# Kernel optimization log

Measured on AMD Instinct MI355X. Metric: run time of the kernel, lower is better.

The kernel has to match this reference:

```python
import jax, jax.numpy as jnp
import numpy as np

B, N, D, H, E = 8, 2048, 128, 256, 524288
EPS = 1e-5

def setup_inputs() -> dict:
    key = jax.random.key(0)
    ks = jax.random.split(key, 16)
    def lin(k, fan_in, shape):
        b = 1.0 / np.sqrt(fan_in)
        return jax.random.uniform(k, shape, jnp.float32, -b, b)
    return {
        'x': jax.random.normal(ks[0], (B, N, 3), jnp.float32),
        'h': jax.random.normal(ks[1], (B, N, D), jnp.float32),
        'edge_indices': jax.random.randint(ks[2], (2, E), 0, B * N, jnp.int64),
        'batch_size': B,
        # filter_net: Linear(1,H) -> SiLU -> Linear(H,D)   (weights stored [in,out])
        'W1': lin(ks[3], 1, (1, H)), 'b1': lin(ks[4], 1, (H,)),
        'W2': lin(ks[5], H, (H, D)), 'b2': lin(ks[6], H, (D,)),
        # update_net: Linear(2D,H) -> LayerNorm(H) -> SiLU -> Linear(H,D)
        'W3': lin(ks[7], 2 * D, (2 * D, H)), 'b3': lin(ks[8], 2 * D, (H,)),
        'gamma': jnp.ones((H,), jnp.float32), 'beta': jnp.zeros((H,), jnp.float32),
        'W4': lin(ks[9], H, (H, D)), 'b4': lin(ks[10], H, (D,)),
    }

def reference(x, h, edge_indices, batch_size, W1, b1, W2, b2, W3, b3, gamma, beta, W4, b4):
    Bn, Nn, Dn = h.shape
    row, col = edge_indices[0], edge_indices[1]
    br, nr = row // Nn, row % Nn
    bc, nc = col // Nn, col % Nn
    x_row = x[br, nr]            # [E,3] gather
    x_col = x[bc, nc]            # [E,3]
    h_col = h[bc, nc]            # [E,D]
    diff = x_row - x_col
    dist = jnp.sqrt(jnp.sum(diff * diff, axis=-1, keepdims=True))  # [E,1]
    # distance-conditioned edge filter MLP
    edge_filters = jax.nn.silu(dist @ W1 + b1) @ W2 + b2           # [E,D]
    messages = h_col * edge_filters                                 # [E,D]
    # scatter-mean into B*N nodes (single-pass sum + count, clamp_min(1))
    n_tot = Bn * Nn
    sums = jax.ops.segment_sum(messages, row, num_segments=n_tot)
    counts = jax.ops.segment_sum(jnp.ones_like(row, dtype=messages.dtype), row, num_segments=n_tot)
    agg = (sums / jnp.maximum(counts, 1.0)[:, None]).reshape(Bn, Nn, Dn)
    # update MLP with LayerNorm
    u = jnp.concatenate([h, agg], axis=-1) @ W3 + b3               # [B,N,H]
    mu = jnp.mean(u, axis=-1, keepdims=True)
    var = jnp.mean((u - mu) ** 2, axis=-1, keepdims=True)
    un = (u - mu) * jax.lax.rsqrt(var + EPS) * gamma + beta
    return jax.nn.silu(un) @ W4 + b4                                # [B,N,D]
```

## Files before the change

kernel.cpp:

```cpp
#include <hip/hip_runtime.h>
#include <hip/hip_fp16.h>
#include <math.h>

#define BN_NODES 16384
#define DIM 128
#define HID 256
#define TK 4096
#define TRANGE 32.0f
#define TSTEP (TRANGE / (float)TK)
#define TINV  ((float)TK / TRANGE)
#define LN_EPS 1e-5f
#define EPB 4096
#define NBINS 1024
#define CAPB 768

typedef _Float16 f16x8 __attribute__((ext_vector_type(8)));
typedef __attribute__((ext_vector_type(4))) float f32x4;
typedef __attribute__((ext_vector_type(2))) float floatx2;
typedef __attribute__((ext_vector_type(8))) unsigned short ushort8v;

__device__ __forceinline__ unsigned short f2h(float f) {
    _Float16 h = (_Float16)f;
    return *(unsigned short*)&h;
}
__device__ __forceinline__ unsigned char f2fp8(float f) {
    unsigned int p = __builtin_amdgcn_cvt_pk_fp8_f32(f, f, 0, false);
    return (unsigned char)(p & 0xFFu);
}

__device__ __forceinline__ void acc8(uint2 q, uint2 tv, float* a) {
    floatx2 h01 = __builtin_amdgcn_cvt_pk_f32_fp8((int)q.x, false);
    floatx2 h23 = __builtin_amdgcn_cvt_pk_f32_fp8((int)q.x, true);
    floatx2 h45 = __builtin_amdgcn_cvt_pk_f32_fp8((int)q.y, false);
    floatx2 h67 = __builtin_amdgcn_cvt_pk_f32_fp8((int)q.y, true);
    floatx2 t01 = __builtin_amdgcn_cvt_pk_f32_fp8((int)tv.x, false);
    floatx2 t23 = __builtin_amdgcn_cvt_pk_f32_fp8((int)tv.x, true);
    floatx2 t45 = __builtin_amdgcn_cvt_pk_f32_fp8((int)tv.y, false);
    floatx2 t67 = __builtin_amdgcn_cvt_pk_f32_fp8((int)tv.y, true);
    a[0] = fmaf(h01[0], t01[0], a[0]);
    a[1] = fmaf(h01[1], t01[1], a[1]);
    a[2] = fmaf(h23[0], t23[0], a[2]);
    a[3] = fmaf(h23[1], t23[1], a[3]);
    a[4] = fmaf(h45[0], t45[0], a[4]);
    a[5] = fmaf(h45[1], t45[1], a[5]);
    a[6] = fmaf(h67[0], t67[0], a[6]);
    a[7] = fmaf(h67[1], t67[1], a[7]);
}

__device__ __forceinline__ void edge_one(const unsigned int* lrec, int idx, int dd,
        const unsigned char* __restrict__ xq,
        const unsigned char* __restrict__ Tb, float* a) {
    unsigned int r0 = lrec[idx];
    int c0 = (int)((r0 >> 12) & 0x3FFFu), k0 = (int)(r0 & 0xFFFu);
    uint2 q0 = *(const uint2*)&xq[c0 * DIM + dd];
    uint2 t0 = *(const uint2*)&Tb[k0 * DIM + dd];
    acc8(q0, t0, a);
}

__global__ __launch_bounds__(256) void prep_kernel(
        const float* __restrict__ W1, const float* __restrict__ b1,
        const float* __restrict__ W2, const float* __restrict__ b2,
        const float* __restrict__ W3, const float* __restrict__ W4,
        const float* __restrict__ h, const int* __restrict__ ei,
        const float* __restrict__ x,
        unsigned char* __restrict__ Tb, unsigned short* __restrict__ w3t,
        unsigned short* __restrict__ w4t, unsigned short* __restrict__ xh,
        unsigned char* __restrict__ xq, int* __restrict__ bin_cursor,
        unsigned int* __restrict__ staging, int nE) {
    __shared__ float smem[8 * 256 + 8 * 128];
    int bid = blockIdx.x, t = threadIdx.x;
    if (bid < 512) {
        float* a    = smem;
        float* part = smem + 8 * 256;
        int k0 = bid * 8;
        float w1 = W1[t], bb = b1[t];
#pragma unroll
        for (int k = 0; k < 8; ++k) {
            float dist = ((float)(k0 + k) + 0.5f) * TSTEP;
            float z = dist * w1 + bb;
            a[k * 256 + t] = z / (1.0f + expf(-z));
        }
        __syncthreads();
        int hg = t >> 7, d = t & 127;
        float acc[8] = {0.f,0.f,0.f,0.f,0.f,0.f,0.f,0.f};
        for (int hh = 0; hh < 128; ++hh) {
            int hidx = hg * 128 + hh;
            float w = W2[hidx * DIM + d];
#pragma unroll
            for (int k = 0; k < 8; ++k) acc[k] += a[k * 256 + hidx] * w;
        }
        if (hg == 1) {
#pragma unroll
            for (int k = 0; k < 8; ++k) part[k * 128 + d] = acc[k];
        }
        __syncthreads();
        if (hg == 0) {
            float bd = b2[d];
#pragma unroll
            for (int k = 0; k < 8; ++k)
                Tb[(k0 + k) * DIM + d] = f2fp8(acc[k] + part[k * 128 + d] + bd);
        }
    } else if (bid < 576) {
        float* s = smem;
        int tid = bid - 512, tr = tid >> 3, tc = tid & 7;
        int lr = t >> 5, lc = t & 31;
#pragma unroll
        for (int rep = 0; rep < 4; ++rep) {
            int k = tr * 32 + rep * 8 + lr, n = tc * 32 + lc;
            s[lc * 33 + rep * 8 + lr] = W3[k * 256 + n];
        }
        __syncthreads();
#pragma unroll
        for (int rep = 0; rep < 4; ++rep) {
            int n = tc * 32 + rep * 8 + lr, k = tr * 32 + lc;
            w3t[n * 256 + k] = f2h(s[(rep * 8 + lr) * 33 + lc]);
        }
    } else if (bid < 608) {
        float* s = smem;
        int tid = bid - 576, tr = tid >> 2, tc = tid & 3;
        int lr = t >> 5, lc = t & 31;
#pragma unroll
        for (int rep = 0; rep < 4; ++rep) {
            int k = tr * 32 + rep * 8 + lr, n = tc * 32 + lc;
            s[lc * 33 + rep * 8 + lr] = W4[k * 128 + n];
        }
        __syncthreads();
#pragma unroll
        for (int rep = 0; rep < 4; ++rep) {
            int n = tc * 32 + rep * 8 + lr, k = tr * 32 + lc;
            w4t[n * 256 + k] = f2h(s[(rep * 8 + lr) * 33 + lc]);
        }
    } else if (bid < 1632) {
        int i0 = (bid - 608) * 2048 + t * 8;
        float4 v0 = *(const float4*)&h[i0];
        float4 v1 = *(const float4*)&h[i0 + 4];
        ushort8v o;
        o[0] = f2h(v0.x); o[1] = f2h(v0.y); o[2] = f2h(v0.z); o[3] = f2h(v0.w);
        o[4] = f2h(v1.x); o[5] = f2h(v1.y); o[6] = f2h(v1.z); o[7] = f2h(v1.w);
        *(ushort8v*)&xh[i0] = o;
        unsigned int q0 = 0, q1 = 0;
        q0 = __builtin_amdgcn_cvt_pk_fp8_f32(v0.x, v0.y, q0, false);
        q0 = __builtin_amdgcn_cvt_pk_fp8_f32(v0.z, v0.w, q0, true);
        q1 = __builtin_amdgcn_cvt_pk_fp8_f32(v1.x, v1.y, q1, false);
        q1 = __builtin_amdgcn_cvt_pk_fp8_f32(v1.z, v1.w, q1, true);
        uint2 qq; qq.x = q0; qq.y = q1;
        *(uint2*)&xq[i0] = qq;
    } else {
        __shared__ int cnt[NBINS];
        __shared__ int pre[NBINS];
        __shared__ int gba[NBINS];
        __shared__ int sc[256];
        __shared__ unsigned int rec[EPB];
        int e0 = (bid - 1632) * EPB;
        int m = min(EPB, nE - e0);
        if (m < 0) m = 0;
#pragma unroll
        for (int j = 0; j < 4; ++j) cnt[j * 256 + t] = 0;
        __syncthreads();
        unsigned int code[16];
        int rk[16], bn[16];
#pragma unroll
        for (int j = 0; j < 16; ++j) {
            int idx = j * 256 + t;
            rk[j] = -1; bn[j] = 0; code[j] = 0;
            if (idx < m) {
                int e = e0 + idx;
                int r = ei[e], c = ei[nE + e];
                code[j] = ((unsigned int)r << 14) | (unsigned int)c;
                bn[j] = r >> 4;
                rk[j] = atomicAdd(&cnt[bn[j]], 1);
            }
        }
        __syncthreads();
        int c4[4], s4 = 0;
#pragma unroll
        for (int j = 0; j < 4; ++j) { c4[j] = cnt[t * 4 + j]; s4 += c4[j]; }
        sc[t] = s4;
        __syncthreads();
        for (int off = 1; off < 256; off <<= 1) {
            int v = (t >= off) ? sc[t - off] : 0;
            __syncthreads();
            sc[t] += v;
            __syncthreads();
        }
        int run = sc[t] - s4;
#pragma unroll
        for (int j = 0; j < 4; ++j) {
            int b = t * 4 + j;
            pre[b] = run; run += c4[j];
            gba[b] = atomicAdd(&bin_cursor[b], c4[j]);
        }
        __syncthreads();
#pragma unroll
        for (int j = 0; j < 16; ++j)
            if (rk[j] >= 0) rec[pre[bn[j]] + rk[j]] = code[j];
        __syncthreads();
        for (int i = t; i < m; i += 256) {
            unsigned int cd = rec[i];
            int b = (int)(cd >> 18);
            int r = (int)(cd >> 14);
            int c = (int)(cd & 0x3FFFu);
            float dx = x[r * 3 + 0] - x[c * 3 + 0];
            float dy = x[r * 3 + 1] - x[c * 3 + 1];
            float dz = x[r * 3 + 2] - x[c * 3 + 2];
            float u = sqrtf(dx * dx + dy * dy + dz * dz) * TINV;
            int k = min((int)u, TK - 1);
            unsigned int o = ((unsigned int)(r & 15) << 26)
                           | ((unsigned int)c << 12) | (unsigned int)k;
            int off = gba[b] + (i - pre[b]);
            if (off < CAPB) staging[b * CAPB + off] = o;
        }
    }
}

__global__ __launch_bounds__(512, 8) void mega_kernel(
        const unsigned int* __restrict__ staging, const int* __restrict__ bin_cursor,
        const unsigned char* __restrict__ Tb, const unsigned char* __restrict__ xq,
        const unsigned short* __restrict__ xh, const unsigned short* __restrict__ w3t,
        const float* __restrict__ b3, const float* __restrict__ gamma,
        const float* __restrict__ beta, const unsigned short* __restrict__ w4t,
        const float* __restrict__ b4, float* __restrict__ out) {
    __shared__ unsigned int lrec[CAPB];
    __shared__ int cnt16[16];
    __shared__ int pref[17];
    __shared__ int cur[16];
    __shared__ __align__(16) unsigned short aggh[16][136];
    __shared__ __align__(16) unsigned short a_lds[16][264];
    __shared__ float part_s[8][16], part_q[8][16];
    __shared__ float tot_mu[16], tot_rs[16];

    int t = threadIdx.x;
    int bin = blockIdx.x;
    int n0 = bin * 16;
    if (t < 16) cnt16[t] = 0;
    __syncthreads();
    int total = min(bin_cursor[bin], CAPB);
    long base = (long)bin * CAPB;

    unsigned int sr0 = 0, sr1 = 0;
    int have0 = (t < total), have1 = (t + 512 < total);
    if (have0) { sr0 = __builtin_nontemporal_load(&staging[base + t]);
                 atomicAdd(&cnt16[sr0 >> 26], 1); }
    if (have1) { sr1 = __builtin_nontemporal_load(&staging[base + t + 512]);
                 atomicAdd(&cnt16[sr1 >> 26], 1); }
    __syncthreads();
    if (t < 16) {
        int c = cnt16[t];
        int s = c;
#pragma unroll
        for (int off = 1; off < 16; off <<= 1) {
            int v = __shfl_up(s, off, 16);
            if (t >= off) s += v;
        }
        pref[t + 1] = s;
        cur[t] = s - c;
        if (t == 0) pref[0] = 0;
    }
    __syncthreads();

    if (have0) { int pos = atomicAdd(&cur[sr0 >> 26], 1); lrec[pos] = sr0; }
    if (have1) { int pos = atomicAdd(&cur[sr1 >> 26], 1); lrec[pos] = sr1; }
    __syncthreads();

    int wid = t >> 6, lane = t & 63;

    {
        int g = lane >> 4, l16 = lane & 15, dd = l16 * 8;
        int node = wid * 2 + (g >> 1);
        int sub = g & 1;
        int off = pref[node], len = pref[node + 1] - off;
        float a[8] = {0.f,0.f,0.f,0.f,0.f,0.f,0.f,0.f};
        int i = sub;
        for (; i + 6 < len; i += 8) {
            unsigned int r0 = lrec[off + i];
            unsigned int r1 = lrec[off + i + 2];
            unsigned int r2 = lrec[off + i + 4];
            unsigned int r3 = lrec[off + i + 6];
            int c0 = (int)((r0 >> 12) & 0x3FFFu), k0 = (int)(r0 & 0xFFFu);
            int c1 = (int)((r1 >> 12) & 0x3FFFu), k1 = (int)(r1 & 0xFFFu);
            int c2 = (int)((r2 >> 12) & 0x3FFFu), k2 = (int)(r2 & 0xFFFu);
            int c3 = (int)((r3 >> 12) & 0x3FFFu), k3 = (int)(r3 & 0xFFFu);
            uint2 q0 = *(const uint2*)&xq[c0 * DIM + dd];
            uint2 t0 = *(const uint2*)&Tb[k0 * DIM + dd];
            uint2 q1 = *(const uint2*)&xq[c1 * DIM + dd];
            uint2 t1 = *(const uint2*)&Tb[k1 * DIM + dd];
            uint2 q2 = *(const uint2*)&xq[c2 * DIM + dd];
            uint2 t2 = *(const uint2*)&Tb[k2 * DIM + dd];
            uint2 q3 = *(const uint2*)&xq[c3 * DIM + dd];
            uint2 t3 = *(const uint2*)&Tb[k3 * DIM + dd];
            acc8(q0, t0, a);
            acc8(q1, t1, a);
            acc8(q2, t2, a);
            acc8(q3, t3, a);
        }
        for (; i < len; i += 2)
            edge_one(lrec, off + i, dd, xq, Tb, a);
#pragma unroll
        for (int r = 0; r < 8; ++r) a[r] += __shfl_xor(a[r], 16, 64);
        if (sub == 0) {
            float inv = 1.0f / (float)max(len, 1);
            ushort8v o;
#pragma unroll
            for (int r = 0; r < 8; ++r) o[r] = f2h(a[r] * inv);
            *(ushort8v*)&aggh[node][dd] = o;
        }
    }
    __syncthreads();

    int wv = wid, q = lane >> 4, l15 = lane & 15;
    f32x4 acc[2];
    acc[0] = (f32x4){0.f, 0.f, 0.f, 0.f};
    acc[1] = (f32x4){0.f, 0.f, 0.f, 0.f};
    for (int kc = 0; kc < 8; ++kc) {
        f16x8 a;
        if (kc < 4) a = *(const f16x8*)&xh[(n0 + l15) * DIM + kc * 32 + q * 8];
        else        a = *(const f16x8*)&aggh[l15][(kc - 4) * 32 + q * 8];
#pragma unroll
        for (int nt = 0; nt < 2; ++nt) {
            f16x8 b = *(const f16x8*)&w3t[(wv * 32 + nt * 16 + l15) * 256 + kc * 32 + q * 8];
            acc[nt] = __builtin_amdgcn_mfma_f32_16x16x32_f16(a, b, acc[nt], 0, 0, 0);
        }
    }

    float b3v[2], gv[2], bvv[2];
#pragma unroll
    for (int nt = 0; nt < 2; ++nt) {
        int col = wv * 32 + nt * 16 + l15;
        b3v[nt] = b3[col]; gv[nt] = gamma[col]; bvv[nt] = beta[col];
    }
    {
        float s_[4], q_[4];
#pragma unroll
        for (int reg = 0; reg < 4; ++reg) {
            float su = 0.f, sq = 0.f;
#pragma unroll
            for (int nt = 0; nt < 2; ++nt) {
                float v = acc[nt][reg] + b3v[nt];
                acc[nt][reg] = v;
                su += v; sq += v * v;
            }
            s_[reg] = su; q_[reg] = sq;
        }
#pragma unroll
        for (int off = 1; off < 16; off <<= 1) {
#pragma unroll
            for (int reg = 0; reg < 4; ++reg) {
                s_[reg] += __shfl_xor(s_[reg], off, 64);
                q_[reg] += __shfl_xor(q_[reg], off, 64);
            }
        }
        if (l15 == 0) {
#pragma unroll
            for (int reg = 0; reg < 4; ++reg) {
                int r = q * 4 + reg;
                part_s[wv][r] = s_[reg];
                part_q[wv][r] = q_[reg];
            }
        }
    }
    __syncthreads();
    if (t < 16) {
        float st = 0.f, qt = 0.f;
#pragma unroll
        for (int w = 0; w < 8; ++w) { st += part_s[w][t]; qt += part_q[w][t]; }
        float mu = st * (1.0f / 256.0f);
        float var = qt * (1.0f / 256.0f) - mu * mu;
        tot_mu[t] = mu;
        tot_rs[t] = rsqrtf(var + LN_EPS);
    }
    __syncthreads();

#pragma unroll
    for (int reg = 0; reg < 4; ++reg) {
        int r = q * 4 + reg;
        float mu = tot_mu[r], rs = tot_rs[r];
#pragma unroll
        for (int nt = 0; nt < 2; ++nt) {
            float un = (acc[nt][reg] - mu) * rs * gv[nt] + bvv[nt];
            float act = un / (1.0f + expf(-un));
            a_lds[r][wv * 32 + nt * 16 + l15] = f2h(act);
        }
    }
    __syncthreads();

    f32x4 acc2 = (f32x4){0.f, 0.f, 0.f, 0.f};
    int col2 = wv * 16 + l15;
    for (int kc = 0; kc < 8; ++kc) {
        f16x8 a = *(const f16x8*)&a_lds[l15][kc * 32 + q * 8];
        f16x8 b = *(const f16x8*)&w4t[col2 * 256 + kc * 32 + q * 8];
        acc2 = __builtin_amdgcn_mfma_f32_16x16x32_f16(a, b, acc2, 0, 0, 0);
    }
    float b4v = b4[col2];
#pragma unroll
    for (int reg = 0; reg < 4; ++reg) {
        int node = n0 + q * 4 + reg;
        __builtin_nontemporal_store(acc2[reg] + b4v, &out[node * DIM + col2]);
    }
}

extern "C" void kernel_launch(void* const* d_in, const int* in_sizes, int n_in,
                              void* d_out, int out_size, void* d_ws, size_t ws_size,
                              hipStream_t stream) {
    const float* x     = (const float*)d_in[0];
    const float* h     = (const float*)d_in[1];
    const int*   ei    = (const int*)d_in[2];
    const float* W1    = (const float*)d_in[4];
    const float* b1    = (const float*)d_in[5];
    const float* W2    = (const float*)d_in[6];
    const float* b2    = (const float*)d_in[7];
    const float* W3    = (const float*)d_in[8];
    const float* b3    = (const float*)d_in[9];
    const float* gamma = (const float*)d_in[10];
    const float* beta  = (const float*)d_in[11];
    const float* W4    = (const float*)d_in[12];
    const float* b4    = (const float*)d_in[13];
    float* out = (float*)d_out;
    int nE = in_sizes[2] / 2;

    char* ws = (char*)d_ws;
    unsigned char*  Tb   = (unsigned char*)ws;  ws += (size_t)TK * DIM;
    unsigned short* w3t  = (unsigned short*)ws; ws += (size_t)HID * HID * 2;
    unsigned short* w4t  = (unsigned short*)ws; ws += (size_t)DIM * HID * 2;
    unsigned short* xh   = (unsigned short*)ws; ws += (size_t)BN_NODES * DIM * 2;
    unsigned char*  xq   = (unsigned char*)ws;  ws += (size_t)BN_NODES * DIM;
    int* bin_cursor = (int*)ws;                 ws += (size_t)NBINS * 4;
    unsigned int* staging = (unsigned int*)ws;  ws += (size_t)NBINS * CAPB * 4;

    int binBlocks = (nE + EPB - 1) / EPB;
    hipMemsetAsync(bin_cursor, 0, (size_t)NBINS * 4, stream);
    prep_kernel<<<1632 + binBlocks, 256, 0, stream>>>(W1, b1, W2, b2, W3, W4, h, ei, x,
                                                      Tb, w3t, w4t, xh, xq,
                                                      bin_cursor, staging, nE);
    mega_kernel<<<NBINS, 512, 0, stream>>>(staging, bin_cursor, Tb, xq, xh,
                                           w3t, b3, gamma, beta, w4t, b4, out);
}
```

Before: 158.4 us.

## Process 32 nodes per block in fused aggregation/update kernel

Bins now cover 32 destination nodes instead of 16, halving the number of mega_kernel blocks. Each block aggregates 32 nodes with one 16-lane group per node, and runs two M-subtiles in the MFMA GEMMs so every W3/W4 fragment loaded is reused across 32 rows. This cuts weight traffic and per-block overhead. In exchange it adds LDS and register pressure, gives each aggregation group a serial edge loop with no split, and the launch config must match the new bin count. The launch code is not shown.

```diff
diff --git a/kernel.cpp b/kernel.cpp
--- a/kernel.cpp
+++ b/kernel.cpp
@@ -11,8 +11,9 @@
 #define TINV  ((float)TK / TRANGE)
 #define LN_EPS 1e-5f
 #define EPB 4096
-#define NBINS 1024
-#define CAPB 768
+#define NBINS 512
+#define NPB 32
+#define CAPB 1280
 
 typedef _Float16 f16x8 __attribute__((ext_vector_type(8)));
 typedef __attribute__((ext_vector_type(4))) float f32x4;
@@ -155,7 +156,7 @@
         int m = min(EPB, nE - e0);
         if (m < 0) m = 0;
 #pragma unroll
-        for (int j = 0; j < 4; ++j) cnt[j * 256 + t] = 0;
+        for (int j = 0; j < 2; ++j) cnt[j * 256 + t] = 0;
         __syncthreads();
         unsigned int code[16];
         int rk[16], bn[16];
@@ -167,15 +168,15 @@
                 int e = e0 + idx;
                 int r = ei[e], c = ei[nE + e];
                 code[j] = ((unsigned int)r << 14) | (unsigned int)c;
-                bn[j] = r >> 4;
+                bn[j] = r >> 5;
                 rk[j] = atomicAdd(&cnt[bn[j]], 1);
             }
         }
         __syncthreads();
-        int c4[4], s4 = 0;
-#pragma unroll
-        for (int j = 0; j < 4; ++j) { c4[j] = cnt[t * 4 + j]; s4 += c4[j]; }
-        sc[t] = s4;
+        int c2[2], s2 = 0;
+#pragma unroll
+        for (int j = 0; j < 2; ++j) { c2[j] = cnt[t * 2 + j]; s2 += c2[j]; }
+        sc[t] = s2;
         __syncthreads();
         for (int off = 1; off < 256; off <<= 1) {
             int v = (t >= off) ? sc[t - off] : 0;
@@ -183,12 +184,12 @@
             sc[t] += v;
             __syncthreads();
         }
-        int run = sc[t] - s4;
-#pragma unroll
-        for (int j = 0; j < 4; ++j) {
-            int b = t * 4 + j;
-            pre[b] = run; run += c4[j];
-            gba[b] = atomicAdd(&bin_cursor[b], c4[j]);
+        int run = sc[t] - s2;
+#pragma unroll
+        for (int j = 0; j < 2; ++j) {
+            int b = t * 2 + j;
+            pre[b] = run; run += c2[j];
+            gba[b] = atomicAdd(&bin_cursor[b], c2[j]);
         }
         __syncthreads();
 #pragma unroll
@@ -197,7 +198,7 @@
         __syncthreads();
         for (int i = t; i < m; i += 256) {
             unsigned int cd = rec[i];
-            int b = (int)(cd >> 18);
+            int b = (int)(cd >> 19);
             int r = (int)(cd >> 14);
             int c = (int)(cd & 0x3FFFu);
             float dx = x[r * 3 + 0] - x[c * 3 + 0];
@@ -205,7 +206,7 @@
             float dz = x[r * 3 + 2] - x[c * 3 + 2];
             float u = sqrtf(dx * dx + dy * dy + dz * dz) * TINV;
             int k = min((int)u, TK - 1);
-            unsigned int o = ((unsigned int)(r & 15) << 26)
+            unsigned int o = ((unsigned int)(r & 31) << 26)
                            | ((unsigned int)c << 12) | (unsigned int)k;
             int off = gba[b] + (i - pre[b]);
             if (off < CAPB) staging[b * CAPB + off] = o;
@@ -221,35 +222,37 @@
         const float* __restrict__ beta, const unsigned short* __restrict__ w4t,
         const float* __restrict__ b4, float* __restrict__ out) {
     __shared__ unsigned int lrec[CAPB];
-    __shared__ int cnt16[16];
-    __shared__ int pref[17];
-    __shared__ int cur[16];
-    __shared__ __align__(16) unsigned short aggh[16][136];
-    __shared__ __align__(16) unsigned short a_lds[16][264];
-    __shared__ float part_s[8][16], part_q[8][16];
-    __shared__ float tot_mu[16], tot_rs[16];
+    __shared__ int cnt32[NPB];
+    __shared__ int pref[NPB + 1];
+    __shared__ int cur[NPB];
+    __shared__ __align__(16) unsigned short aggh[NPB][136];
+    __shared__ __align__(16) unsigned short a_lds[NPB][264];
+    __shared__ float part_s[8][NPB], part_q[8][NPB];
+    __shared__ float tot_mu[NPB], tot_rs[NPB];
 
     int t = threadIdx.x;
     int bin = blockIdx.x;
-    int n0 = bin * 16;
-    if (t < 16) cnt16[t] = 0;
+    int n0 = bin * NPB;
+    if (t < NPB) cnt32[t] = 0;
     __syncthreads();
     int total = min(bin_cursor[bin], CAPB);
     long base = (long)bin * CAPB;
 
-    unsigned int sr0 = 0, sr1 = 0;
-    int have0 = (t < total), have1 = (t + 512 < total);
+    unsigned int sr0 = 0, sr1 = 0, sr2 = 0;
+    int have0 = (t < total), have1 = (t + 512 < total), have2 = (t + 1024 < total);
     if (have0) { sr0 = __builtin_nontemporal_load(&staging[base + t]);
-                 atomicAdd(&cnt16[sr0 >> 26], 1); }
+                 atomicAdd(&cnt32[sr0 >> 26], 1); }
     if (have1) { sr1 = __builtin_nontemporal_load(&staging[base + t + 512]);
-                 atomicAdd(&cnt16[sr1 >> 26], 1); }
-    __syncthreads();
-    if (t < 16) {
-        int c = cnt16[t];
+                 atomicAdd(&cnt32[sr1 >> 26], 1); }
+    if (have2) { sr2 = __builtin_nontemporal_load(&staging[base + t + 1024]);
+                 atomicAdd(&cnt32[sr2 >> 26], 1); }
+    __syncthreads();
+    if (t < NPB) {
+        int c = cnt32[t];
         int s = c;
 #pragma unroll
-        for (int off = 1; off < 16; off <<= 1) {
-            int v = __shfl_up(s, off, 16);
+        for (int off = 1; off < NPB; off <<= 1) {
+            int v = __shfl_up(s, off, NPB);
             if (t >= off) s += v;
         }
         pref[t + 1] = s;
@@ -260,22 +263,22 @@
 
     if (have0) { int pos = atomicAdd(&cur[sr0 >> 26], 1); lrec[pos] = sr0; }
     if (have1) { int pos = atomicAdd(&cur[sr1 >> 26], 1); lrec[pos] = sr1; }
+    if (have2) { int pos = atomicAdd(&cur[sr2 >> 26], 1); lrec[pos] = sr2; }
     __syncthreads();
 
     int wid = t >> 6, lane = t & 63;
 
     {
         int g = lane >> 4, l16 = lane & 15, dd = l16 * 8;
-        int node = wid * 2 + (g >> 1);
-        int sub = g & 1;
+        int node = wid * 4 + g;
         int off = pref[node], len = pref[node + 1] - off;
         float a[8] = {0.f,0.f,0.f,0.f,0.f,0.f,0.f,0.f};
-        int i = sub;
-        for (; i + 6 < len; i += 8) {
+        int i = 0;
+        for (; i + 3 < len; i += 4) {
             unsigned int r0 = lrec[off + i];
-            unsigned int r1 = lrec[off + i + 2];
-            unsigned int r2 = lrec[off + i + 4];
-            unsigned int r3 = lrec[off + i + 6];
+            unsigned int r1 = lrec[off + i + 1];
+            unsigned int r2 = lrec[off + i + 2];
+            unsigned int r3 = lrec[off + i + 3];
             int c0 = (int)((r0 >> 12) & 0x3FFFu), k0 = (int)(r0 & 0xFFFu);
             int c1 = (int)((r1 >> 12) & 0x3FFFu), k1 = (int)(r1 & 0xFFFu);
             int c2 = (int)((r2 >> 12) & 0x3FFFu), k2 = (int)(r2 & 0xFFFu);
@@ -293,32 +296,36 @@
             acc8(q2, t2, a);
             acc8(q3, t3, a);
         }
-        for (; i < len; i += 2)
+        for (; i < len; ++i)
             edge_one(lrec, off + i, dd, xq, Tb, a);
-#pragma unroll
-        for (int r = 0; r < 8; ++r) a[r] += __shfl_xor(a[r], 16, 64);
-        if (sub == 0) {
-            float inv = 1.0f / (float)max(len, 1);
-            ushort8v o;
-#pragma unroll
-            for (int r = 0; r < 8; ++r) o[r] = f2h(a[r] * inv);
-            *(ushort8v*)&aggh[node][dd] = o;
-        }
+        float inv = 1.0f / (float)max(len, 1);
+        ushort8v o;
+#pragma unroll
+        for (int r = 0; r < 8; ++r) o[r] = f2h(a[r] * inv);
+        *(ushort8v*)&aggh[node][dd] = o;
     }
     __syncthreads();
 
     int wv = wid, q = lane >> 4, l15 = lane & 15;
-    f32x4 acc[2];
-    acc[0] = (f32x4){0.f, 0.f, 0.f, 0.f};
-    acc[1] = (f32x4){0.f, 0.f, 0.f, 0.f};
+    f32x4 acc[2][2];
+#pragma unroll
+    for (int ms = 0; ms < 2; ++ms)
+#pragma unroll
+        for (int nt = 0; nt < 2; ++nt) acc[ms][nt] = (f32x4){0.f, 0.f, 0.f, 0.f};
     for (int kc = 0; kc < 8; ++kc) {
-        f16x8 a;
-        if (kc < 4) a = *(const f16x8*)&xh[(n0 + l15) * DIM + kc * 32 + q * 8];
-        else        a = *(const f16x8*)&aggh[l15][(kc - 4) * 32 + q * 8];
+        f16x8 a0, a1;
+        if (kc < 4) {
+            a0 = *(const f16x8*)&xh[(n0 + l15) * DIM + kc * 32 + q * 8];
+            a1 = *(const f16x8*)&xh[(n0 + 16 + l15) * DIM + kc * 32 + q * 8];
+        } else {
+            a0 = *(const f16x8*)&aggh[l15][(kc - 4) * 32 + q * 8];
+            a1 = *(const f16x8*)&aggh[16 + l15][(kc - 4) * 32 + q * 8];
+        }
 #pragma unroll
         for (int nt = 0; nt < 2; ++nt) {
             f16x8 b = *(const f16x8*)&w3t[(wv * 32 + nt * 16 + l15) * 256 + kc * 32 + q * 8];
-            acc[nt] = __builtin_amdgcn_mfma_f32_16x16x32_f16(a, b, acc[nt], 0, 0, 0);
+            acc[0][nt] = __builtin_amdgcn_mfma_f32_16x16x32_f16(a0, b, acc[0][nt], 0, 0, 0);
+            acc[1][nt] = __builtin_amdgcn_mfma_f32_16x16x32_f16(a1, b, acc[1][nt], 0, 0, 0);
         }
     }
 
@@ -328,15 +335,16 @@
         int col = wv * 32 + nt * 16 + l15;
         b3v[nt] = b3[col]; gv[nt] = gamma[col]; bvv[nt] = beta[col];
     }
-    {
+#pragma unroll
+    for (int ms = 0; ms < 2; ++ms) {
         float s_[4], q_[4];
 #pragma unroll
         for (int reg = 0; reg < 4; ++reg) {
             float su = 0.f, sq = 0.f;
 #pragma unroll
             for (int nt = 0; nt < 2; ++nt) {
-                float v = acc[nt][reg] + b3v[nt];
-                acc[nt][reg] = v;
+                float v = acc[ms][nt][reg] + b3v[nt];
+                acc[ms][nt][reg] = v;
                 su += v; sq += v * v;
             }
             s_[reg] = su; q_[reg] = sq;
@@ -352,14 +360,14 @@
         if (l15 == 0) {
 #pragma unroll
             for (int reg = 0; reg < 4; ++reg) {
-                int r = q * 4 + reg;
+                int r = ms * 16 + q * 4 + reg;
                 part_s[wv][r] = s_[reg];
                 part_q[wv][r] = q_[reg];
             }
         }
     }
     __syncthreads();
-    if (t < 16) {
+    if (t < NPB) {
         float st = 0.f, qt = 0.f;
 #pragma unroll
         for (int w = 0; w < 8; ++w) { st += part_s[w][t]; qt += part_q[w][t]; }
@@ -371,30 +379,40 @@
     __syncthreads();
 
 #pragma unroll
-    for (int reg = 0; reg < 4; ++reg) {
-        int r = q * 4 + reg;
-        float mu = tot_mu[r], rs = tot_rs[r];
-#pragma unroll
-        for (int nt = 0; nt < 2; ++nt) {
-            float un = (acc[nt][reg] - mu) * rs * gv[nt] + bvv[nt];
-            float act = un / (1.0f + expf(-un));
-            a_lds[r][wv * 32 + nt * 16 + l15] = f2h(act);
-        }
-    }
-    __syncthreads();
-
-    f32x4 acc2 = (f32x4){0.f, 0.f, 0.f, 0.f};
+    for (int ms = 0; ms < 2; ++ms) {
+#pragma unroll
+        for (int reg = 0; reg < 4; ++reg) {
+            int r = ms * 16 + q * 4 + reg;
+            float mu = tot_mu[r], rs = tot_rs[r];
+#pragma unroll
+            for (int nt = 0; nt < 2; ++nt) {
+                float un = (acc[ms][nt][reg] - mu) * rs * gv[nt] + bvv[nt];
+                float act = un / (1.0f + expf(-un));
+                a_lds[r][wv * 32 + nt * 16 + l15] = f2h(act);
+            }
+        }
+    }
+    __syncthreads();
+
+    f32x4 acc2[2];
+    acc2[0] = (f32x4){0.f, 0.f, 0.f, 0.f};
+    acc2[1] = (f32x4){0.f, 0.f, 0.f, 0.f};
     int col2 = wv * 16 + l15;
     for (int kc = 0; kc < 8; ++kc) {
-        f16x8 a = *(const f16x8*)&a_lds[l15][kc * 32 + q * 8];
+        f16x8 a0 = *(const f16x8*)&a_lds[l15][kc * 32 + q * 8];
+        f16x8 a1 = *(const f16x8*)&a_lds[16 + l15][kc * 32 + q * 8];
         f16x8 b = *(const f16x8*)&w4t[col2 * 256 + kc * 32 + q * 8];
-        acc2 = __builtin_amdgcn_mfma_f32_16x16x32_f16(a, b, acc2, 0, 0, 0);
+        acc2[0] = __builtin_amdgcn_mfma_f32_16x16x32_f16(a0, b, acc2[0], 0, 0, 0);
+        acc2[1] = __builtin_amdgcn_mfma_f32_16x16x32_f16(a1, b, acc2[1], 0, 0, 0);
     }
     float b4v = b4[col2];
 #pragma unroll
-    for (int reg = 0; reg < 4; ++reg) {
-        int node = n0 + q * 4 + reg;
-        __builtin_nontemporal_store(acc2[reg] + b4v, &out[node * DIM + col2]);
+    for (int ms = 0; ms < 2; ++ms) {
+#pragma unroll
+        for (int reg = 0; reg < 4; ++reg) {
+            int node = n0 + ms * 16 + q * 4 + reg;
+            __builtin_nontemporal_store(acc2[ms][reg] + b4v, &out[node * DIM + col2]);
+        }
     }
 }
 
```

New measurement: 147.4 us. 6.9% less time.
